# Optimization experiments

Hardware: AMD Instinct MI355X
Metric: run time of the kernel (lower is better)

## Reference

```python
import jax, jax.numpy as jnp
import numpy as np

# output_shape = (batch, channels, ny, nx)
B, C, NY, NX = 16, 64, 400, 400
NV_PER_BATCH = 12000  # non-empty pillars per frame (typical PointPillars)


def setup_inputs() -> dict:
    rng = np.random.default_rng(0)
    # unique pillar cells per batch -> deterministic scatter (matches torch last-write)
    cells = np.stack([rng.choice(NY * NX, NV_PER_BATCH, replace=False) for _ in range(B)])  # (B, NV)
    b_col = np.repeat(np.arange(B), NV_PER_BATCH)
    y = (cells // NX).reshape(-1)
    x = (cells % NX).reshape(-1)
    z = np.zeros_like(x)
    batched_indices = jnp.asarray(np.stack([b_col, z, y, x], axis=1), dtype=jnp.int32)  # (N, 4)
    voxel_features = jax.random.normal(jax.random.key(0), (B * NV_PER_BATCH, C), dtype=jnp.float32)
    return {"voxel_features": voxel_features, "batched_indices": batched_indices}


def reference(voxel_features, batched_indices):
    # fused global flat index: (batch, y, x) -> b*ny*nx + y*nx + x
    b = batched_indices[:, 0].astype(jnp.int32)
    y = batched_indices[:, 2].astype(jnp.int32)
    x = batched_indices[:, 3].astype(jnp.int32)
    flat = b * (NY * NX) + y * NX + x  # (N,)
    canvas = jnp.zeros((B * NY * NX, voxel_features.shape[1]), dtype=voxel_features.dtype)
    canvas = canvas.at[flat].set(voxel_features, unique_indices=True)
    # (B*NY*NX, C) -> (B, C, NY, NX)
    return canvas.reshape(B, NY, NX, -1).transpose(0, 3, 1, 2)
```

## Files before the change

kernel.cpp:

```cpp
#include <hip/hip_runtime.h>


constexpr int BATCH = 16;
constexpr int CH    = 64;
constexpr int NYD   = 400;
constexpr int NXD   = 400;
constexpr int NYNX  = NYD * NXD;
constexpr int SLABS = 8;
constexpr int CPS   = CH / SLABS;
constexpr int TILE  = 1024;

typedef float f4 __attribute__((ext_vector_type(4)));

__global__ void scatter_map_kernel(const int4* __restrict__ idx,
                                   unsigned short* __restrict__ map, int n, int nv) {
    int i = blockIdx.x * blockDim.x + threadIdx.x;
    if (i < n) {
        int4 v = idx[i];
        map[v.x * NYNX + v.z * NXD + v.w] = (unsigned short)(i - v.x * nv);
    }
}

__global__ __launch_bounds__(256)
void gather_kernel(const float* __restrict__ feat,
                   const unsigned short* __restrict__ map,
                   float* __restrict__ out, int nv) {
    const int b  = blockIdx.y;
    const int yx = blockIdx.x * TILE + threadIdx.x * 4;
    if (yx >= NYNX) return;

    const unsigned short* mapb  = map  + (size_t)b * NYNX;
    const float*          featb = feat + ((size_t)b * nv) * CH;
    float*                outb  = out  + (size_t)b * CH * NYNX + yx;
    const f4 z4 = {0.f, 0.f, 0.f, 0.f};

    const ushort4 m = *reinterpret_cast<const ushort4*>(mapb + yx);
    const unsigned short js[4] = {m.x, m.y, m.z, m.w};

    f4 fA[4][2], fB[4][2];

    #pragma unroll
    for (int cc = 0; cc < 4; ++cc) {
        if (js[cc] != 0xFFFFu) {
            const f4* src = reinterpret_cast<const f4*>(featb + (size_t)js[cc] * CH);
            fA[cc][0] = src[0];
            fA[cc][1] = src[1];
        } else {
            fA[cc][0] = z4;
            fA[cc][1] = z4;
        }
    }

    #pragma unroll
    for (int s = 0; s < SLABS; ++s) {
        f4 (*cur)[2] = (s & 1) ? fB : fA;
        f4 (*nxt)[2] = (s & 1) ? fA : fB;

        if (s + 1 < SLABS) {
            #pragma unroll
            for (int cc = 0; cc < 4; ++cc) {
                if (js[cc] != 0xFFFFu) {
                    const f4* src = reinterpret_cast<const f4*>(
                        featb + (size_t)js[cc] * CH + (s + 1) * CPS);
                    nxt[cc][0] = src[0];
                    nxt[cc][1] = src[1];
                } else {
                    nxt[cc][0] = z4;
                    nxt[cc][1] = z4;
                }
            }
        }

        float* outs = outb + (size_t)s * CPS * NYNX;
        #pragma unroll
        for (int k = 0; k < 2; ++k) {
            f4 r0 = {cur[0][k].x, cur[1][k].x, cur[2][k].x, cur[3][k].x};
            f4 r1 = {cur[0][k].y, cur[1][k].y, cur[2][k].y, cur[3][k].y};
            f4 r2 = {cur[0][k].z, cur[1][k].z, cur[2][k].z, cur[3][k].z};
            f4 r3 = {cur[0][k].w, cur[1][k].w, cur[2][k].w, cur[3][k].w};
            __builtin_nontemporal_store(r0, reinterpret_cast<f4*>(outs + (size_t)(4 * k + 0) * NYNX));
            __builtin_nontemporal_store(r1, reinterpret_cast<f4*>(outs + (size_t)(4 * k + 1) * NYNX));
            __builtin_nontemporal_store(r2, reinterpret_cast<f4*>(outs + (size_t)(4 * k + 2) * NYNX));
            __builtin_nontemporal_store(r3, reinterpret_cast<f4*>(outs + (size_t)(4 * k + 3) * NYNX));
        }
    }
}

__global__ void zero_kernel(float4* __restrict__ out, int n4) {
    int i = blockIdx.x * blockDim.x + threadIdx.x;
    if (i < n4) out[i] = make_float4(0.f, 0.f, 0.f, 0.f);
}

__global__ void direct_scatter_kernel(const float* __restrict__ feat,
                                      const int4* __restrict__ idx,
                                      float* __restrict__ out, int n) {
    int i = blockIdx.x * (blockDim.x / CH) + threadIdx.x / CH;
    int c = threadIdx.x % CH;
    if (i < n) {
        int4 v = idx[i];
        out[(size_t)(v.x * CH + c) * NYNX + v.z * NXD + v.w] = feat[(size_t)i * CH + c];
    }
}

extern "C" void kernel_launch(void* const* d_in, const int* in_sizes, int n_in,
                              void* d_out, int out_size, void* d_ws, size_t ws_size,
                              hipStream_t stream) {
    const float* feat = (const float*)d_in[0];
    const int4*  idx  = (const int4*)d_in[1];
    float*       out  = (float*)d_out;
    const int n  = in_sizes[1] / 4;
    const int nv = n / BATCH;

    const size_t map_bytes = (size_t)BATCH * NYNX * sizeof(unsigned short);
    if (ws_size >= map_bytes && nv < 0xFFFF) {
        unsigned short* map = (unsigned short*)d_ws;
        (void)hipMemsetAsync(map, 0xFF, map_bytes, stream);
        scatter_map_kernel<<<(n + 255) / 256, 256, 0, stream>>>(idx, map, n, nv);
        dim3 grid((NYNX + TILE - 1) / TILE, BATCH, 1);
        gather_kernel<<<grid, 256, 0, stream>>>(feat, map, out, nv);
    } else {
        int n4 = out_size / 4;
        zero_kernel<<<(n4 + 255) / 256, 256, 0, stream>>>((float4*)out, n4);
        direct_scatter_kernel<<<(n + 3) / 4, 256, 0, stream>>>(feat, idx, out, n);
    }
}
```

Measured before the change: 688.6 us.

## Remap gather blocks per XCD, drop register double-buffer, raise occupancy

```diff
diff --git a/kernel.cpp b/kernel.cpp
--- a/kernel.cpp
+++ b/kernel.cpp
@@ -9,6 +9,9 @@
 constexpr int SLABS = 8;
 constexpr int CPS   = CH / SLABS;
 constexpr int TILE  = 1024;
+constexpr int XB    = (NYNX + TILE - 1) / TILE;
+constexpr int NXCD  = 8;
+constexpr int BPX   = BATCH / NXCD;
 
 typedef float f4 __attribute__((ext_vector_type(4)));
 
@@ -21,12 +24,15 @@
     }
 }
 
-__global__ __launch_bounds__(256)
+__global__ __launch_bounds__(256, 8)
 void gather_kernel(const float* __restrict__ feat,
                    const unsigned short* __restrict__ map,
                    float* __restrict__ out, int nv) {
-    const int b  = blockIdx.y;
-    const int yx = blockIdx.x * TILE + threadIdx.x * 4;
+    const int xcd = blockIdx.x & (NXCD - 1);
+    const int idx = blockIdx.x >> 3;
+    const int sub = (idx >= XB) ? 1 : 0;
+    const int b   = xcd * BPX + sub;
+    const int yx  = (idx - sub * XB) * TILE + threadIdx.x * 4;
     if (yx >= NYNX) return;
 
     const unsigned short* mapb  = map  + (size_t)b * NYNX;
@@ -35,49 +41,39 @@
     const f4 z4 = {0.f, 0.f, 0.f, 0.f};
 
     const ushort4 m = *reinterpret_cast<const ushort4*>(mapb + yx);
-    const unsigned short js[4] = {m.x, m.y, m.z, m.w};
-
-    f4 fA[4][2], fB[4][2];
-
-    #pragma unroll
-    for (int cc = 0; cc < 4; ++cc) {
-        if (js[cc] != 0xFFFFu) {
-            const f4* src = reinterpret_cast<const f4*>(featb + (size_t)js[cc] * CH);
-            fA[cc][0] = src[0];
-            fA[cc][1] = src[1];
-        } else {
-            fA[cc][0] = z4;
-            fA[cc][1] = z4;
+    bool live[4];
+    int  off[4];
+    {
+        const unsigned short js[4] = {m.x, m.y, m.z, m.w};
+        #pragma unroll
+        for (int cc = 0; cc < 4; ++cc) {
+            live[cc] = (js[cc] != 0xFFFFu);
+            off[cc]  = (int)js[cc] * CH;
         }
     }
 
-    #pragma unroll
+    #pragma unroll 1
     for (int s = 0; s < SLABS; ++s) {
-        f4 (*cur)[2] = (s & 1) ? fB : fA;
-        f4 (*nxt)[2] = (s & 1) ? fA : fB;
-
-        if (s + 1 < SLABS) {
-            #pragma unroll
-            for (int cc = 0; cc < 4; ++cc) {
-                if (js[cc] != 0xFFFFu) {
-                    const f4* src = reinterpret_cast<const f4*>(
-                        featb + (size_t)js[cc] * CH + (s + 1) * CPS);
-                    nxt[cc][0] = src[0];
-                    nxt[cc][1] = src[1];
-                } else {
-                    nxt[cc][0] = z4;
-                    nxt[cc][1] = z4;
-                }
+        f4 f[4][2];
+        #pragma unroll
+        for (int cc = 0; cc < 4; ++cc) {
+            if (live[cc]) {
+                const f4* src = reinterpret_cast<const f4*>(featb + off[cc] + s * CPS);
+                f[cc][0] = src[0];
+                f[cc][1] = src[1];
+            } else {
+                f[cc][0] = z4;
+                f[cc][1] = z4;
             }
         }
 
         float* outs = outb + (size_t)s * CPS * NYNX;
         #pragma unroll
         for (int k = 0; k < 2; ++k) {
-            f4 r0 = {cur[0][k].x, cur[1][k].x, cur[2][k].x, cur[3][k].x};
-            f4 r1 = {cur[0][k].y, cur[1][k].y, cur[2][k].y, cur[3][k].y};
-            f4 r2 = {cur[0][k].z, cur[1][k].z, cur[2][k].z, cur[3][k].z};
-            f4 r3 = {cur[0][k].w, cur[1][k].w, cur[2][k].w, cur[3][k].w};
+            f4 r0 = {f[0][k].x, f[1][k].x, f[2][k].x, f[3][k].x};
+            f4 r1 = {f[0][k].y, f[1][k].y, f[2][k].y, f[3][k].y};
+            f4 r2 = {f[0][k].z, f[1][k].z, f[2][k].z, f[3][k].z};
+            f4 r3 = {f[0][k].w, f[1][k].w, f[2][k].w, f[3][k].w};
             __builtin_nontemporal_store(r0, reinterpret_cast<f4*>(outs + (size_t)(4 * k + 0) * NYNX));
             __builtin_nontemporal_store(r1, reinterpret_cast<f4*>(outs + (size_t)(4 * k + 1) * NYNX));
             __builtin_nontemporal_store(r2, reinterpret_cast<f4*>(outs + (size_t)(4 * k + 2) * NYNX));
@@ -116,8 +112,7 @@
         unsigned short* map = (unsigned short*)d_ws;
         (void)hipMemsetAsync(map, 0xFF, map_bytes, stream);
         scatter_map_kernel<<<(n + 255) / 256, 256, 0, stream>>>(idx, map, n, nv);
-        dim3 grid((NYNX + TILE - 1) / TILE, BATCH, 1);
-        gather_kernel<<<grid, 256, 0, stream>>>(feat, map, out, nv);
+        gather_kernel<<<dim3(XB * BATCH), 256, 0, stream>>>(feat, map, out, nv);
     } else {
         int n4 = out_size / 4;
         zero_kernel<<<(n4 + 255) / 256, 256, 0, stream>>>((float4*)out, n4);
```

New measurement: 698.0 us. No clear change (+1.4%).
